# Kernel tuning notes

Hardware: AMD Instinct MI355X
Metric: run time of the kernel (lower is better)

Reference implementation:

```python
import jax, jax.numpy as jnp
import numpy as np

HEAD_DIM = 128
NUM_Q_HEADS = 32
NUM_KV_HEADS = 8
HIDDEN = HEAD_DIM * NUM_Q_HEADS  # 4096
ROPE_BASE = 10000.0


def setup_inputs() -> dict:
    key = jax.random.key(0)
    k1, k2, k3, k4, k5 = jax.random.split(key, 5)
    B, S = 1, 2048
    scale = 0.02  # keep activations sane given integer-valued x
    input_ids = jax.random.randint(k5, (B, S), 0, 100, dtype=jnp.int64) if jax.config.jax_enable_x64 else jax.random.randint(k5, (B, S), 0, 100, dtype=jnp.int32)
    position_ids = (jnp.arange(B * S).reshape(B, S) % S).astype(input_ids.dtype)
    Wq = jax.random.normal(k1, (HIDDEN, NUM_Q_HEADS * HEAD_DIM), dtype=jnp.float32) * scale
    Wk = jax.random.normal(k2, (HIDDEN, NUM_KV_HEADS * HEAD_DIM), dtype=jnp.float32) * scale
    Wv = jax.random.normal(k3, (HIDDEN, NUM_KV_HEADS * HEAD_DIM), dtype=jnp.float32) * scale
    Wo = jax.random.normal(k4, (NUM_Q_HEADS * HEAD_DIM, HIDDEN), dtype=jnp.float32) * scale
    return {"input_ids": input_ids, "position_ids": position_ids,
            "Wq": Wq, "Wk": Wk, "Wv": Wv, "Wo": Wo}


def _rotate_half(x):
    x1, x2 = jnp.split(x, 2, axis=-1)
    return jnp.concatenate([-x2, x1], axis=-1)


def _cos_sin(position_ids):
    # standard RoPE cos/sin, shape [B, S, 1, head_dim]
    inv_freq = 1.0 / (ROPE_BASE ** (jnp.arange(0, HEAD_DIM, 2, dtype=jnp.float32) / HEAD_DIM))
    ang = position_ids.astype(jnp.float32)[..., None] * inv_freq  # [B,S,d/2]
    cos = jnp.concatenate([jnp.cos(ang), jnp.cos(ang)], axis=-1)[:, :, None, :]
    sin = jnp.concatenate([jnp.sin(ang), jnp.sin(ang)], axis=-1)[:, :, None, :]
    return cos, sin


def reference(input_ids, position_ids, Wq, Wk, Wv, Wo):
    B, S = input_ids.shape
    # x = input_ids broadcast to hidden_size (as in the torch model)
    x = jnp.broadcast_to(input_ids[..., None].astype(jnp.float32), (B, S, HIDDEN))
    q = (x @ Wq).reshape(B, S, NUM_Q_HEADS, HEAD_DIM)
    k = (x @ Wk).reshape(B, S, NUM_KV_HEADS, HEAD_DIM)
    v = (x @ Wv).reshape(B, S, NUM_KV_HEADS, HEAD_DIM)
    cos, sin = _cos_sin(position_ids)
    q = q * cos + _rotate_half(q) * sin
    k = k * cos + _rotate_half(k) * sin
    # GQA: group q heads over kv heads
    G = NUM_Q_HEADS // NUM_KV_HEADS
    qg = q.reshape(B, S, NUM_KV_HEADS, G, HEAD_DIM)
    scores = jnp.einsum('bqhgd,bkhd->bhgqk', qg, k) / jnp.sqrt(jnp.float32(HEAD_DIM))
    causal = jnp.tril(jnp.ones((S, S), dtype=bool))  # [S_q, S_k]
    scores = jnp.where(causal, scores, -jnp.inf)
    attn = jax.nn.softmax(scores, axis=-1)
    out = jnp.einsum('bhgqk,bkhd->bqhgd', attn, v).reshape(B, S, NUM_Q_HEADS * HEAD_DIM)
    return out @ Wo
```

## Files before the change

### kernel.cpp

```cpp
#include <hip/hip_runtime.h>
#include <math.h>


#define HID 4096
#define NQH 32
#define NKVH 8
#define HD 128
#define CHQ 128
#define TS 64
#define RSQRT_HD 0.08838834764831845f
#define LOG2E    1.4426950408889634f

__device__ __forceinline__ void colsum_seq(const float* __restrict__ W,
                                           float* __restrict__ P,
                                           int nth4, int u) {
    const float4* b = reinterpret_cast<const float4*>(W);
    float ax = 0.f, ay = 0.f, az = 0.f, aw = 0.f;
#pragma unroll
    for (int k = 0; k < 32; k += 16) {
        float4 tt[16];
#pragma unroll
        for (int i = 0; i < 16; ++i) tt[i] = b[(size_t)(k + i) * nth4 + u];
#pragma unroll
        for (int i = 0; i < 16; i += 4) {
            ax += (tt[i].x + tt[i+1].x) + (tt[i+2].x + tt[i+3].x);
            ay += (tt[i].y + tt[i+1].y) + (tt[i+2].y + tt[i+3].y);
            az += (tt[i].z + tt[i+1].z) + (tt[i+2].z + tt[i+3].z);
            aw += (tt[i].w + tt[i+1].w) + (tt[i+2].w + tt[i+3].w);
        }
    }
    reinterpret_cast<float4*>(P)[u] = make_float4(ax, ay, az, aw);
}

__global__ __launch_bounds__(256) void k_part(
        const int* __restrict__ ids,
        const float* __restrict__ Wq, const float* __restrict__ Wk,
        const float* __restrict__ Wv,
        float* __restrict__ Pq, float* __restrict__ Pk, float* __restrict__ Pv,
        float* __restrict__ cp, double* __restrict__ Tc,
        double* __restrict__ Ts, int S) {
    int t = blockIdx.x;
    int tid = threadIdx.x;
    int nxb = S >> 8;
    int trigT = 64 * nxb;
    if (t < trigT) {
        int j = t / nxb, xb = t - j * nxb;
        int dlt = xb * 256 + tid;
        double f = (double)(float)(1.0 / pow(10000.0, (double)j / 64.0));
        double sv, cv;
        sincos((double)dlt * f, &sv, &cv);
        Tc[(size_t)j * S + dlt] = cv;
        Ts[(size_t)j * S + dlt] = sv;
        if (j == 0) cp[dlt] = (float)ids[dlt];
    } else if (t < trigT + 512) {
        colsum_seq(Wq, Pq, 512 * 256, (t - trigT) * 256 + tid);
    } else if (t < trigT + 640) {
        colsum_seq(Wk, Pk, 128 * 256, (t - trigT - 512) * 256 + tid);
    } else {
        colsum_seq(Wv, Pv, 128 * 256, (t - trigT - 640) * 256 + tid);
    }
}

__global__ __launch_bounds__(256) void k_dtab(
        const float* __restrict__ Pq, const float* __restrict__ Pk,
        const double* __restrict__ Tc, const double* __restrict__ Ts,
        float* __restrict__ D, int S) {
    __shared__ float sq[128], sk[128];
    __shared__ double p[64], q[64];
    int nxb = S >> 8;
    int hg = blockIdx.x / nxb, xb = blockIdx.x - hg * nxb, h = hg >> 2;
    int tid = threadIdx.x;
    if (tid < 128) {
        const float* base = Pq + hg * HD + tid;
        float a = 0.f;
#pragma unroll 16
        for (int dep = 0; dep < CHQ; ++dep) a += base[(size_t)dep * 4096];
        sq[tid] = a;
    } else {
        int d = tid - 128;
        const float* base = Pk + h * HD + d;
        float a = 0.f;
#pragma unroll 16
        for (int dep = 0; dep < CHQ; ++dep) a += base[(size_t)dep * 1024];
        sk[d] = a;
    }
    __syncthreads();
    if (tid < 64) {
        double a1 = sq[tid], a2 = sq[tid + 64];
        double b1 = sk[tid], b2 = sk[tid + 64];
        p[tid] = a1 * b1 + a2 * b2;
        q[tid] = a2 * b1 - a1 * b2;
    }
    __syncthreads();
    int dlt = xb * 256 + tid;
    const double* tc = Tc + dlt;
    const double* ts = Ts + dlt;
    double acc = 0.0;
#pragma unroll 8
    for (int j = 0; j < 64; ++j)
        acc += p[j] * tc[(size_t)j * S] - q[j] * ts[(size_t)j * S];
    D[(size_t)hg * S + dlt] = (float)acc;
}

__global__ __launch_bounds__(256) void k_fuse(
        const int* __restrict__ ids, const float* __restrict__ cp,
        const float* __restrict__ D, const float* __restrict__ Pv,
        const float* __restrict__ Wo, float* __restrict__ Mp,
        float* __restrict__ A, int S) {
    int t = blockIdx.x;
    int tid = threadIdx.x;
    if (t < 512) {
        __shared__ float part[8][32];
        __shared__ float svs[32];
        int sl = t & 3, x = (t >> 2) & 3, hg = t >> 4, h = hg >> 2;
        {
            int j = tid & 31, g = tid >> 5;
            const float* base = Pv + (size_t)(g * 16) * 1024 + h * HD + sl * 32 + j;
            float a = 0.f;
#pragma unroll
            for (int dep = 0; dep < 16; ++dep) a += base[(size_t)dep * 1024];
            part[g][j] = a;
        }
        __syncthreads();
        if (tid < 32) {
            float a = 0.f;
#pragma unroll
            for (int g = 0; g < 8; ++g) a += part[g][tid];
            svs[tid] = a;
        }
        __syncthreads();
        int dbase = hg * HD + sl * 32;
        int i4 = x * 256 + tid;
        const float4* b = reinterpret_cast<const float4*>(Wo);
        float ax = 0.f, ay = 0.f, az = 0.f, aw = 0.f;
#pragma unroll
        for (int half = 0; half < 32; half += 16) {
            size_t pbase = (size_t)(dbase + half) * (HID / 4) + i4;
            float4 tt[16];
#pragma unroll
            for (int i = 0; i < 16; ++i) tt[i] = b[pbase + (size_t)i * (HID / 4)];
#pragma unroll
            for (int i = 0; i < 16; ++i) {
                float ss = svs[half + i];
                ax += ss * tt[i].x; ay += ss * tt[i].y;
                az += ss * tt[i].z; aw += ss * tt[i].w;
            }
        }
        reinterpret_cast<float4*>(Mp)[((size_t)sl * NQH + hg) * (HID / 4) + i4] =
            make_float4(ax, ay, az, aw);
        return;
    }
    int u = t - 512;
    int tile = u >> 5;
    int hg = u & 31;
    int s0 = S - TS - tile * TS;
    int w = tid >> 6, lane = tid & 63;
    int sl = s0 + lane;
    float csl = (float)ids[sl] * (RSQRT_HD * LOG2E);
    const float* Drow = D + (size_t)hg * S + sl;

    int n = s0 + TS;
    int q4 = ((n + 15) >> 4) << 2;
    int k = w * q4;
    int k1 = (k + q4 < n) ? k + q4 : n;
    int lim = (k1 < s0 + 1) ? k1 : s0 + 1;

    float tm = -1e30f;
    float mz = csl * tm;
    float se = 0.f, sp = 0.f;

    for (; k + 8 <= lim; k += 8) {
        float4 cv0 = *reinterpret_cast<const float4*>(cp + k);
        float4 cv1 = *reinterpret_cast<const float4*>(cp + k + 4);
        float d0 = Drow[-k],     d1 = Drow[-(k+1)], d2 = Drow[-(k+2)], d3 = Drow[-(k+3)];
        float d4 = Drow[-(k+4)], d5 = Drow[-(k+5)], d6 = Drow[-(k+6)], d7 = Drow[-(k+7)];
        float t0 = cv0.x * d0, t1 = cv0.y * d1, t2 = cv0.z * d2, t3 = cv0.w * d3;
        float t4 = cv1.x * d4, t5 = cv1.y * d5, t6 = cv1.z * d6, t7 = cv1.w * d7;
        float m8 = fmaxf(fmaxf(fmaxf(t0, t1), fmaxf(t2, t3)),
                         fmaxf(fmaxf(t4, t5), fmaxf(t6, t7)));
        if (!__all(m8 <= tm)) {
            float ntm = fmaxf(tm, m8);
            float nmz = csl * ntm;
            float r = __builtin_amdgcn_exp2f(fminf(mz - nmz, 0.f));
            se *= r; sp *= r; tm = ntm; mz = nmz;
        }
        float e0 = __builtin_amdgcn_exp2f(fmaf(csl, t0, -mz));
        float e1 = __builtin_amdgcn_exp2f(fmaf(csl, t1, -mz));
        float e2 = __builtin_amdgcn_exp2f(fmaf(csl, t2, -mz));
        float e3 = __builtin_amdgcn_exp2f(fmaf(csl, t3, -mz));
        float e4 = __builtin_amdgcn_exp2f(fmaf(csl, t4, -mz));
        float e5 = __builtin_amdgcn_exp2f(fmaf(csl, t5, -mz));
        float e6 = __builtin_amdgcn_exp2f(fmaf(csl, t6, -mz));
        float e7 = __builtin_amdgcn_exp2f(fmaf(csl, t7, -mz));
        se += ((e0 + e1) + (e2 + e3)) + ((e4 + e5) + (e6 + e7));
        sp = fmaf(e0, cv0.x, sp); sp = fmaf(e1, cv0.y, sp);
        sp = fmaf(e2, cv0.z, sp); sp = fmaf(e3, cv0.w, sp);
        sp = fmaf(e4, cv1.x, sp); sp = fmaf(e5, cv1.y, sp);
        sp = fmaf(e6, cv1.z, sp); sp = fmaf(e7, cv1.w, sp);
    }
    for (; k + 4 <= lim; k += 4) {
        float4 cv = *reinterpret_cast<const float4*>(cp + k);
        float d0 = Drow[-k], d1 = Drow[-(k+1)], d2 = Drow[-(k+2)], d3 = Drow[-(k+3)];
        float t0 = cv.x * d0, t1 = cv.y * d1, t2 = cv.z * d2, t3 = cv.w * d3;
        float m4 = fmaxf(fmaxf(t0, t1), fmaxf(t2, t3));
        if (!__all(m4 <= tm)) {
            float ntm = fmaxf(tm, m4);
            float nmz = csl * ntm;
            float r = __builtin_amdgcn_exp2f(fminf(mz - nmz, 0.f));
            se *= r; sp *= r; tm = ntm; mz = nmz;
        }
        float e0 = __builtin_amdgcn_exp2f(fmaf(csl, t0, -mz));
        float e1 = __builtin_amdgcn_exp2f(fmaf(csl, t1, -mz));
        float e2 = __builtin_amdgcn_exp2f(fmaf(csl, t2, -mz));
        float e3 = __builtin_amdgcn_exp2f(fmaf(csl, t3, -mz));
        se += (e0 + e1) + (e2 + e3);
        sp = fmaf(e0, cv.x, sp); sp = fmaf(e1, cv.y, sp);
        sp = fmaf(e2, cv.z, sp); sp = fmaf(e3, cv.w, sp);
    }
    for (; k < k1; k += 4) {
        float4 cv = *reinterpret_cast<const float4*>(cp + k);
        float d0 = Drow[-k], d1 = Drow[-(k+1)], d2 = Drow[-(k+2)], d3 = Drow[-(k+3)];
        bool v0 = (k + 0 <= sl) && (k + 0 < k1);
        bool v1 = (k + 1 <= sl) && (k + 1 < k1);
        bool v2 = (k + 2 <= sl) && (k + 2 < k1);
        bool v3 = (k + 3 <= sl) && (k + 3 < k1);
        float t0 = v0 ? cv.x * d0 : -1e30f;
        float t1 = v1 ? cv.y * d1 : -1e30f;
        float t2 = v2 ? cv.z * d2 : -1e30f;
        float t3 = v3 ? cv.w * d3 : -1e30f;
        float m4 = fmaxf(fmaxf(t0, t1), fmaxf(t2, t3));
        if (!__all(m4 <= tm)) {
            float ntm = fmaxf(tm, m4);
            float nmz = csl * ntm;
            float r = __builtin_amdgcn_exp2f(fminf(mz - nmz, 0.f));
            se *= r; sp *= r; tm = ntm; mz = nmz;
        }
        float e0 = __builtin_amdgcn_exp2f(fmaf(csl, t0, -mz)); e0 = v0 ? e0 : 0.f;
        float e1 = __builtin_amdgcn_exp2f(fmaf(csl, t1, -mz)); e1 = v1 ? e1 : 0.f;
        float e2 = __builtin_amdgcn_exp2f(fmaf(csl, t2, -mz)); e2 = v2 ? e2 : 0.f;
        float e3 = __builtin_amdgcn_exp2f(fmaf(csl, t3, -mz)); e3 = v3 ? e3 : 0.f;
        se += (e0 + e1) + (e2 + e3);
        sp = fmaf(e0, cv.x, sp); sp = fmaf(e1, cv.y, sp);
        sp = fmaf(e2, cv.z, sp); sp = fmaf(e3, cv.w, sp);
    }

    __shared__ float lm[4][TS], ls[4][TS], lp[4][TS];
    lm[w][lane] = mz; ls[w][lane] = se; lp[w][lane] = sp;
    __syncthreads();
    if (tid < TS) {
        float m0 = lm[0][tid], m1 = lm[1][tid], m2 = lm[2][tid], m3 = lm[3][tid];
        float mm = fmaxf(fmaxf(m0, m1), fmaxf(m2, m3));
        float r0 = __builtin_amdgcn_exp2f(fminf(m0 - mm, 0.f));
        float r1 = __builtin_amdgcn_exp2f(fminf(m1 - mm, 0.f));
        float r2 = __builtin_amdgcn_exp2f(fminf(m2 - mm, 0.f));
        float r3 = __builtin_amdgcn_exp2f(fminf(m3 - mm, 0.f));
        float seT = ls[0][tid] * r0 + ls[1][tid] * r1 + ls[2][tid] * r2 + ls[3][tid] * r3;
        float spT = lp[0][tid] * r0 + lp[1][tid] * r1 + lp[2][tid] * r2 + lp[3][tid] * r3;
        A[(size_t)hg * S + s0 + tid] = spT / seT;
    }
}

__global__ void k_out(const float* __restrict__ A, const float* __restrict__ Mp,
                      float* __restrict__ out, int S) {
    __shared__ float a[512];
    int tid = threadIdx.x;
    int s0 = blockIdx.y * 16;
    for (int v = tid; v < 512; v += 256) {
        int hg = v >> 4, r = v & 15;
        a[r * NQH + hg] = A[(size_t)hg * S + s0 + r];
    }
    __syncthreads();
    int i = blockIdx.x * 256 + tid;
    const int Q = NQH * HID;
    float acc[16];
#pragma unroll
    for (int rr = 0; rr < 16; ++rr) acc[rr] = 0.f;
    for (int hg = 0; hg < NQH; ++hg) {
        size_t base = (size_t)hg * HID + i;
        float mv = (Mp[base] + Mp[base + Q]) + (Mp[base + 2 * Q] + Mp[base + 3 * Q]);
#pragma unroll
        for (int rr = 0; rr < 16; ++rr) acc[rr] += a[rr * NQH + hg] * mv;
    }
#pragma unroll
    for (int rr = 0; rr < 16; ++rr)
        out[(size_t)(s0 + rr) * HID + i] = acc[rr];
}

extern "C" void kernel_launch(void* const* d_in, const int* in_sizes, int n_in,
                              void* d_out, int out_size, void* d_ws, size_t ws_size,
                              hipStream_t stream) {
    const int*   ids = (const int*)d_in[0];
    const float* Wq  = (const float*)d_in[2];
    const float* Wk  = (const float*)d_in[3];
    const float* Wv  = (const float*)d_in[4];
    const float* Wo  = (const float*)d_in[5];
    float* out = (float*)d_out;
    const int S = in_sizes[0];
    const int nxb = S >> 8;

    float* ws = (float*)d_ws;
    float* Pq = ws;
    float* Pk = Pq + (size_t)CHQ * NQH * HD;
    float* Pv = Pk + (size_t)CHQ * NKVH * HD;
    float* D  = Pv + (size_t)CHQ * NKVH * HD;
    float* cp = D + (size_t)NQH * S;
    float* A  = cp + S;
    double* Tc = (double*)(A + (size_t)NQH * S);
    double* Ts = Tc + (size_t)64 * S;
    float* Mp = (float*)Tc;

    k_part<<<64 * nxb + 512 + 128 + 128, 256, 0, stream>>>(
        ids, Wq, Wk, Wv, Pq, Pk, Pv, cp, Tc, Ts, S);
    k_dtab<<<NQH * nxb, 256, 0, stream>>>(Pq, Pk, Tc, Ts, D, S);
    k_fuse<<<512 + (S / TS) * NQH, 256, 0, stream>>>(ids, cp, D, Pv, Wo, Mp, A, S);
    k_out<<<dim3(HID / 256, S / 16), 256, 0, stream>>>(A, Mp, out, S);
}
```

Measured before the change: 89.95 us.

## Reorder fused kernel blocks and re-split the Wo projection into 256 wider blocks

```diff
diff --git a/kernel.cpp b/kernel.cpp
--- a/kernel.cpp
+++ b/kernel.cpp
@@ -109,48 +109,59 @@
         float* __restrict__ A, int S) {
     int t = blockIdx.x;
     int tid = threadIdx.x;
-    if (t < 512) {
-        __shared__ float part[8][32];
-        __shared__ float svs[32];
-        int sl = t & 3, x = (t >> 2) & 3, hg = t >> 4, h = hg >> 2;
+    int nAlpha = (S / TS) * NQH;
+    __shared__ float lm[4][TS], ls[4][TS], lp[4][TS];
+    __shared__ float part[16][16], svs[16];
+    if (t >= nAlpha) {
+        int m = t - nAlpha;
+        int hg = m >> 3, sl = m & 7, h = hg >> 2;
+        int d0 = sl * 16;
         {
-            int j = tid & 31, g = tid >> 5;
-            const float* base = Pv + (size_t)(g * 16) * 1024 + h * HD + sl * 32 + j;
+            int v = tid & 15, g = tid >> 4;
+            const float* base = Pv + (size_t)(g * 8) * 1024 + h * HD + d0 + v;
             float a = 0.f;
 #pragma unroll
-            for (int dep = 0; dep < 16; ++dep) a += base[(size_t)dep * 1024];
-            part[g][j] = a;
+            for (int dep = 0; dep < 8; ++dep) a += base[(size_t)dep * 1024];
+            part[g][v] = a;
         }
         __syncthreads();
-        if (tid < 32) {
+        if (tid < 16) {
             float a = 0.f;
 #pragma unroll
-            for (int g = 0; g < 8; ++g) a += part[g][tid];
+            for (int g = 0; g < 16; ++g) a += part[g][tid];
             svs[tid] = a;
         }
         __syncthreads();
-        int dbase = hg * HD + sl * 32;
-        int i4 = x * 256 + tid;
         const float4* b = reinterpret_cast<const float4*>(Wo);
-        float ax = 0.f, ay = 0.f, az = 0.f, aw = 0.f;
-#pragma unroll
-        for (int half = 0; half < 32; half += 16) {
-            size_t pbase = (size_t)(dbase + half) * (HID / 4) + i4;
-            float4 tt[16];
-#pragma unroll
-            for (int i = 0; i < 16; ++i) tt[i] = b[pbase + (size_t)i * (HID / 4)];
-#pragma unroll
-            for (int i = 0; i < 16; ++i) {
-                float ss = svs[half + i];
-                ax += ss * tt[i].x; ay += ss * tt[i].y;
-                az += ss * tt[i].z; aw += ss * tt[i].w;
-            }
-        }
-        reinterpret_cast<float4*>(Mp)[((size_t)sl * NQH + hg) * (HID / 4) + i4] =
-            make_float4(ax, ay, az, aw);
+        size_t rowbase = (size_t)(hg * HD + d0) * (HID / 4) + tid;
+        float a0x=0.f,a0y=0.f,a0z=0.f,a0w=0.f, a1x=0.f,a1y=0.f,a1z=0.f,a1w=0.f;
+        float a2x=0.f,a2y=0.f,a2z=0.f,a2w=0.f, a3x=0.f,a3y=0.f,a3z=0.f,a3w=0.f;
+#pragma unroll
+        for (int rr = 0; rr < 16; rr += 2) {
+            size_t p0 = rowbase + (size_t)rr * (HID / 4);
+            float4 t0 = b[p0],        t1 = b[p0 + 256];
+            float4 t2 = b[p0 + 512],  t3 = b[p0 + 768];
+            float4 u0 = b[p0 + 1024], u1 = b[p0 + 1280];
+            float4 u2 = b[p0 + 1536], u3 = b[p0 + 1792];
+            float s0 = svs[rr], s1 = svs[rr + 1];
+            a0x += s0*t0.x + s1*u0.x; a0y += s0*t0.y + s1*u0.y;
+            a0z += s0*t0.z + s1*u0.z; a0w += s0*t0.w + s1*u0.w;
+            a1x += s0*t1.x + s1*u1.x; a1y += s0*t1.y + s1*u1.y;
+            a1z += s0*t1.z + s1*u1.z; a1w += s0*t1.w + s1*u1.w;
+            a2x += s0*t2.x + s1*u2.x; a2y += s0*t2.y + s1*u2.y;
+            a2z += s0*t2.z + s1*u2.z; a2w += s0*t2.w + s1*u2.w;
+            a3x += s0*t3.x + s1*u3.x; a3y += s0*t3.y + s1*u3.y;
+            a3z += s0*t3.z + s1*u3.z; a3w += s0*t3.w + s1*u3.w;
+        }
+        float4* mp4 = reinterpret_cast<float4*>(Mp) +
+                      ((size_t)(sl * NQH + hg)) * (HID / 4) + tid;
+        mp4[0]    = make_float4(a0x, a0y, a0z, a0w);
+        mp4[256]  = make_float4(a1x, a1y, a1z, a1w);
+        mp4[512]  = make_float4(a2x, a2y, a2z, a2w);
+        mp4[768]  = make_float4(a3x, a3y, a3z, a3w);
         return;
     }
-    int u = t - 512;
+    int u = t;
     int tile = u >> 5;
     int hg = u & 31;
     int s0 = S - TS - tile * TS;
@@ -244,7 +255,6 @@
         sp = fmaf(e2, cv.z, sp); sp = fmaf(e3, cv.w, sp);
     }
 
-    __shared__ float lm[4][TS], ls[4][TS], lp[4][TS];
     lm[w][lane] = mz; ls[w][lane] = se; lp[w][lane] = sp;
     __syncthreads();
     if (tid < TS) {
@@ -277,7 +287,8 @@
     for (int rr = 0; rr < 16; ++rr) acc[rr] = 0.f;
     for (int hg = 0; hg < NQH; ++hg) {
         size_t base = (size_t)hg * HID + i;
-        float mv = (Mp[base] + Mp[base + Q]) + (Mp[base + 2 * Q] + Mp[base + 3 * Q]);
+        float mv = ((Mp[base] + Mp[base + Q]) + (Mp[base + 2*Q] + Mp[base + 3*Q]))
+                 + ((Mp[base + 4*Q] + Mp[base + 5*Q]) + (Mp[base + 6*Q] + Mp[base + 7*Q]));
 #pragma unroll
         for (int rr = 0; rr < 16; ++rr) acc[rr] += a[rr * NQH + hg] * mv;
     }
@@ -312,6 +323,6 @@
     k_part<<<64 * nxb + 512 + 128 + 128, 256, 0, stream>>>(
         ids, Wq, Wk, Wv, Pq, Pk, Pv, cp, Tc, Ts, S);
     k_dtab<<<NQH * nxb, 256, 0, stream>>>(Pq, Pk, Tc, Ts, D, S);
-    k_fuse<<<512 + (S / TS) * NQH, 256, 0, stream>>>(ids, cp, D, Pv, Wo, Mp, A, S);
+    k_fuse<<<(S / TS) * NQH + 256, 256, 0, stream>>>(ids, cp, D, Pv, Wo, Mp, A, S);
     k_out<<<dim3(HID / 256, S / 16), 256, 0, stream>>>(A, Mp, out, S);
 }
```

Result: no change. 90.83 us (+1.0%).
